# Optimization experiments

Hardware: AMD Instinct MI355X
Metric: run time of the kernel (lower is better)

## Reference

```python
import jax, jax.numpy as jnp
import numpy as np

NV, NC = 100000, 50000        # num variables, num constraints
DV, DC = 8, 16                # padded neighbor-list widths
DIN, DH = 32, 128             # init_input_dim, output_dim (=init_output_dim)
NUM_LAYERS = 3                # aggregate loop runs num_layers-1 times
DCAT = 2 * DH + DIN           # input_dim of fc_variable/fc_constraint


def setup_inputs() -> dict:
    key = jax.random.key(0)
    ks = jax.random.split(key, 10)
    w = lambda k, shape: (jax.random.normal(k, shape, jnp.float32) * 0.05)
    return {
        "x": jax.random.normal(ks[0], (NV + NC, DIN), jnp.float32),
        "var_constr_index": jax.random.randint(ks[1], (NV, DV), 0, NC, dtype=jnp.int32),
        "constr_var_index": jax.random.randint(ks[2], (NC, DC), 0, NV, dtype=jnp.int32),
        "W_init_v": w(ks[3], (DIN, DH)), "b_init_v": jnp.zeros((DH,), jnp.float32),
        "W_init_c": w(ks[4], (DIN, DH)), "b_init_c": jnp.zeros((DH,), jnp.float32),
        "W_var": w(ks[5], (DCAT, DH)), "b_var": jnp.zeros((DH,), jnp.float32),
        "W_con": w(ks[6], (DCAT, DH)), "b_con": jnp.zeros((DH,), jnp.float32),
        "W_q": w(ks[7], (2 * DH, 1)), "b_q": jnp.zeros((1,), jnp.float32),
    }


def reference(x, var_constr_index, constr_var_index,
              W_init_v, b_init_v, W_init_c, b_init_c,
              W_var, b_var, W_con, b_con, W_q, b_q):
    nv = var_constr_index.shape[0]
    xv, xc = x[:nv], x[nv:]
    # layer zero init (fc_init_variables / fc_init_constraints)
    v = xv @ W_init_v + b_init_v          # [NV, DH]
    c = xc @ W_init_c + b_init_c          # [NC, DH]
    # message-passing layers: both updates read OLD v and OLD c
    for _ in range(1, NUM_LAYERS):
        agg_c = jnp.sum(v[constr_var_index], axis=1)   # [NC, DH] gather+sum over variable neighbors
        agg_v = jnp.sum(c[var_constr_index], axis=1)   # [NV, DH] gather+sum over constraint neighbors
        c_new = jnp.concatenate([agg_c, c, xc], axis=1) @ W_con + b_con
        v_new = jnp.concatenate([agg_v, v, xv], axis=1) @ W_var + b_var
        c, v = c_new, v_new
    # embedding_Q: global sum of variable features, broadcast, concat, linear
    g = jnp.sum(v, axis=0)                             # [DH]
    q_in = jnp.concatenate([jnp.broadcast_to(g, v.shape), v], axis=1)  # [NV, 2*DH]
    return q_in @ W_q + b_q                            # [NV, 1]
```

## Files before the change

kernel.cpp:

```cpp
#include <hip/hip_runtime.h>

#define NV 100000
#define NC 50000
#define DVAR 8
#define DCON 16

using short8 = __attribute__((ext_vector_type(8))) short;
using f32x4  = __attribute__((ext_vector_type(4))) float;

__device__ __forceinline__ unsigned short f2bf(float f) {
    union { float f; unsigned int u; } v; v.f = f;
    return (unsigned short)((v.u + 0x7fffu + ((v.u >> 16) & 1u)) >> 16);
}
__device__ __forceinline__ float bflo(unsigned int u) {
    union { unsigned int u; float f; } v; v.u = u << 16; return v.f;
}
__device__ __forceinline__ float bfhi(unsigned int u) {
    union { unsigned int u; float f; } v; v.u = u & 0xffff0000u; return v.f;
}

__global__ __launch_bounds__(256) void pack_kernel(
    const float* __restrict__ Wvar, const float* __restrict__ Wcon,
    const float* __restrict__ Wiv,  const float* __restrict__ Wic,
    unsigned short* __restrict__ WbVar, unsigned short* __restrict__ WbCon,
    unsigned short* __restrict__ WbIv,  unsigned short* __restrict__ WbIc,
    float* __restrict__ S)
{
    const int tid = blockIdx.x * 256 + threadIdx.x;
    for (int i = tid; i < 9 * 128 * 32; i += gridDim.x * 256) {
        int s = i >> 12, rem = i & 4095, c = rem >> 5, k = rem & 31;
        int src = (s * 32 + k) * 128 + c;
        WbVar[i] = f2bf(Wvar[src]);
        WbCon[i] = f2bf(Wcon[src]);
    }
    for (int i = tid; i < 128 * 32; i += gridDim.x * 256) {
        int c = i >> 5, k = i & 31;
        int src = k * 128 + c;
        WbIv[i] = f2bf(Wiv[src]);
        WbIc[i] = f2bf(Wic[src]);
    }
    if (tid == 0) S[0] = 0.f;
}

__global__ __launch_bounds__(256) void init_mfma(
    const float* __restrict__ x,
    const unsigned short* __restrict__ Wb,
    const float* __restrict__ bias,
    unsigned short* __restrict__ hout, int M)
{
    const int t = threadIdx.x;
    const int lane = t & 63;
    const int w = t >> 6;
    const int lrow = lane & 15;
    const int lg = lane >> 4;
    const int wrow0 = blockIdx.x * 64 + w * 16;
    int arow = wrow0 + lrow;
    int arowc = arow < M ? arow : M - 1;

    const float4* xp = (const float4*)(x + (size_t)arowc * 32 + lg * 8);
    float4 xa = xp[0], xb = xp[1];
    short8 afr;
    afr[0] = (short)f2bf(xa.x); afr[1] = (short)f2bf(xa.y);
    afr[2] = (short)f2bf(xa.z); afr[3] = (short)f2bf(xa.w);
    afr[4] = (short)f2bf(xb.x); afr[5] = (short)f2bf(xb.y);
    afr[6] = (short)f2bf(xb.z); afr[7] = (short)f2bf(xb.w);

    #pragma unroll
    for (int ct = 0; ct < 8; ++ct) {
        int c = ct * 16 + lrow;
        short8 bfr = *(const short8*)(Wb + (size_t)c * 32 + lg * 8);
        f32x4 acc = {0.f, 0.f, 0.f, 0.f};
        acc = __builtin_amdgcn_mfma_f32_16x16x32_bf16(afr, bfr, acc, 0, 0, 0);
        float bv = bias[c];
        #pragma unroll
        for (int r = 0; r < 4; ++r) {
            int orow = wrow0 + lg * 4 + r;
            if (orow < M) hout[(size_t)orow * 128 + c] = f2bf(acc[r] + bv);
        }
    }
}

template<int DEG, bool FINAL>
__global__ __launch_bounds__(256) void layer_mfma(
    const unsigned short* hself,
    const unsigned short* __restrict__ hnb,
    const float* __restrict__ xself,
    const int* __restrict__ idx,
    const unsigned short* __restrict__ Wb,
    const float* __restrict__ bias,
    unsigned short* hout,
    const float* __restrict__ Wq, float* __restrict__ S, float* __restrict__ dotout,
    int M)
{
    __shared__ unsigned short A[64 * 136];
    __shared__ float red[4];
    const int t = threadIdx.x;
    const int r0 = blockIdx.x * 64;

    {
        const int part = t & 15;
        const int gr = t >> 4;
        #pragma unroll
        for (int rr = gr; rr < 64; rr += 16) {
            int row = r0 + rr;
            int rowc = row < M ? row : M - 1;
            int nb[DEG];
            #pragma unroll
            for (int d4 = 0; d4 < DEG / 4; ++d4)
                *(int4*)(&nb[d4 * 4]) = *(const int4*)(idx + (size_t)rowc * DEG + d4 * 4);
            float a0=0.f,a1=0.f,a2=0.f,a3=0.f,a4=0.f,a5=0.f,a6=0.f,a7=0.f;
            #pragma unroll
            for (int d = 0; d < DEG; ++d) {
                const uint4 q = *(const uint4*)(hnb + (size_t)nb[d] * 128 + part * 8);
                a0 += bflo(q.x); a1 += bfhi(q.x);
                a2 += bflo(q.y); a3 += bfhi(q.y);
                a4 += bflo(q.z); a5 += bfhi(q.z);
                a6 += bflo(q.w); a7 += bfhi(q.w);
            }
            uint4 o;
            o.x = (unsigned)f2bf(a0) | ((unsigned)f2bf(a1) << 16);
            o.y = (unsigned)f2bf(a2) | ((unsigned)f2bf(a3) << 16);
            o.z = (unsigned)f2bf(a4) | ((unsigned)f2bf(a5) << 16);
            o.w = (unsigned)f2bf(a6) | ((unsigned)f2bf(a7) << 16);
            *(uint4*)(&A[rr * 136 + part * 8]) = o;
        }
    }
    __syncthreads();

    const int lane = t & 63;
    const int w = t >> 6;
    const int lrow = lane & 15;
    const int lg = lane >> 4;
    const int wrow0 = r0 + w * 16;
    int arow = wrow0 + lrow;
    int arowc = arow < M ? arow : M - 1;

    f32x4 acc[8];
    #pragma unroll
    for (int ct = 0; ct < 8; ++ct) acc[ct] = (f32x4){0.f, 0.f, 0.f, 0.f};

    #pragma unroll
    for (int s = 0; s < 9; ++s) {
        short8 afr;
        if (s < 4) {
            afr = *(const short8*)(&A[(w * 16 + lrow) * 136 + s * 32 + lg * 8]);
        } else if (s < 8) {
            afr = *(const short8*)(hself + (size_t)arowc * 128 + (s - 4) * 32 + lg * 8);
        } else {
            const float4* xp = (const float4*)(xself + (size_t)arowc * 32 + lg * 8);
            float4 xa = xp[0], xb = xp[1];
            afr[0] = (short)f2bf(xa.x); afr[1] = (short)f2bf(xa.y);
            afr[2] = (short)f2bf(xa.z); afr[3] = (short)f2bf(xa.w);
            afr[4] = (short)f2bf(xb.x); afr[5] = (short)f2bf(xb.y);
            afr[6] = (short)f2bf(xb.z); afr[7] = (short)f2bf(xb.w);
        }
        #pragma unroll
        for (int ct = 0; ct < 8; ++ct) {
            short8 bfr = *(const short8*)(Wb + ((size_t)s * 128 + ct * 16 + lrow) * 32 + lg * 8);
            acc[ct] = __builtin_amdgcn_mfma_f32_16x16x32_bf16(afr, bfr, acc[ct], 0, 0, 0);
        }
    }

    if (!FINAL) {
        #pragma unroll
        for (int ct = 0; ct < 8; ++ct) {
            int c = ct * 16 + lrow;
            float bv = bias[c];
            #pragma unroll
            for (int r = 0; r < 4; ++r) {
                int orow = wrow0 + lg * 4 + r;
                if (orow < M) hout[(size_t)orow * 128 + c] = f2bf(acc[ct][r] + bv);
            }
        }
    } else {
        float d0[4] = {0.f, 0.f, 0.f, 0.f};
        float d1[4] = {0.f, 0.f, 0.f, 0.f};
        #pragma unroll
        for (int ct = 0; ct < 8; ++ct) {
            int c = ct * 16 + lrow;
            float bv = bias[c];
            float wq0 = Wq[c];
            float wq1 = Wq[128 + c];
            #pragma unroll
            for (int r = 0; r < 4; ++r) {
                int orow = wrow0 + lg * 4 + r;
                float val = (orow < M) ? (acc[ct][r] + bv) : 0.f;
                d0[r] += val * wq0;
                d1[r] += val * wq1;
            }
        }
        #pragma unroll
        for (int r = 0; r < 4; ++r) {
            d0[r] += __shfl_xor(d0[r], 1); d0[r] += __shfl_xor(d0[r], 2);
            d0[r] += __shfl_xor(d0[r], 4); d0[r] += __shfl_xor(d0[r], 8);
            d1[r] += __shfl_xor(d1[r], 1); d1[r] += __shfl_xor(d1[r], 2);
            d1[r] += __shfl_xor(d1[r], 4); d1[r] += __shfl_xor(d1[r], 8);
        }
        if (lrow == 0) {
            #pragma unroll
            for (int r = 0; r < 4; ++r) {
                int orow = wrow0 + lg * 4 + r;
                if (orow < M) dotout[orow] = d1[r];
            }
        }
        float tot = d0[0] + d0[1] + d0[2] + d0[3];
        tot += __shfl_xor(tot, 16);
        tot += __shfl_xor(tot, 32);
        if (lane == 0) red[w] = tot;
        __syncthreads();
        if (t == 0) atomicAdd(S, red[0] + red[1] + red[2] + red[3]);
    }
}

__global__ __launch_bounds__(256) void addout_kernel(
    float* __restrict__ outp, const float* __restrict__ S,
    const float* __restrict__ bq, int n)
{
    int i = blockIdx.x * 256 + threadIdx.x;
    if (i < n) outp[i] = outp[i] + S[0] + bq[0];
}

extern "C" void kernel_launch(void* const* d_in, const int* in_sizes, int n_in,
                              void* d_out, int out_size, void* d_ws, size_t ws_size,
                              hipStream_t stream)
{
    const float* x    = (const float*)d_in[0];
    const int*   vci  = (const int*)  d_in[1];
    const int*   cvi  = (const int*)  d_in[2];
    const float* Wiv  = (const float*)d_in[3];
    const float* biv  = (const float*)d_in[4];
    const float* Wic  = (const float*)d_in[5];
    const float* bic  = (const float*)d_in[6];
    const float* Wvar = (const float*)d_in[7];
    const float* bvar = (const float*)d_in[8];
    const float* Wcon = (const float*)d_in[9];
    const float* bcon = (const float*)d_in[10];
    const float* Wq   = (const float*)d_in[11];
    const float* bq   = (const float*)d_in[12];
    float* outp = (float*)d_out;

    unsigned short* us = (unsigned short*)d_ws;
    size_t o = 0;
    unsigned short* vA    = us + o; o += (size_t)NV * 128;
    unsigned short* cA    = us + o; o += (size_t)NC * 128;
    unsigned short* cB    = us + o; o += (size_t)NC * 128;
    unsigned short* WbVar = us + o; o += 9 * 128 * 32;
    unsigned short* WbCon = us + o; o += 9 * 128 * 32;
    unsigned short* WbIv  = us + o; o += 128 * 32;
    unsigned short* WbIc  = us + o; o += 128 * 32;
    float* S = (float*)(us + o);

    const float* xc = x + (size_t)NV * 32;

    pack_kernel<<<144, 256, 0, stream>>>(Wvar, Wcon, Wiv, Wic, WbVar, WbCon, WbIv, WbIc, S);
    init_mfma<<<(NV + 63) / 64, 256, 0, stream>>>(x,  WbIv, biv, vA, NV);
    init_mfma<<<(NC + 63) / 64, 256, 0, stream>>>(xc, WbIc, bic, cA, NC);
    layer_mfma<DCON, false><<<(NC + 63) / 64, 256, 0, stream>>>(
        cA, vA, xc, cvi, WbCon, bcon, cB, nullptr, nullptr, nullptr, NC);
    layer_mfma<DVAR, false><<<(NV + 63) / 64, 256, 0, stream>>>(
        vA, cA, x, vci, WbVar, bvar, vA, nullptr, nullptr, nullptr, NV);
    layer_mfma<DVAR, true><<<(NV + 63) / 64, 256, 0, stream>>>(
        vA, cB, x, vci, WbVar, bvar, nullptr, Wq, S, outp, NV);
    addout_kernel<<<(NV + 255) / 256, 256, 0, stream>>>(outp, S, bq, NV);
}
```

Before: 285.3 us.

## Gather neighbor aggregation directly into MFMA register fragments, dropping LDS staging

Each lane now gathers and sums neighbor rows straight into the register layout of its MFMA A-fragment, so the shared-memory tile and the block-wide barrier are no longer needed. Self and input-feature fragments are loaded up front, and their MFMAs are issued before the aggregated fragments so the matrix work can overlap the gather latency. Each lane issues four 16-byte loads per neighbor instead of one, and holding 32 float accumulators raises register pressure, which may lower occupancy.

```diff
diff --git a/kernel.cpp b/kernel.cpp
--- a/kernel.cpp
+++ b/kernel.cpp
@@ -92,68 +92,71 @@
     const float* __restrict__ Wq, float* __restrict__ S, float* __restrict__ dotout,
     int M)
 {
-    __shared__ unsigned short A[64 * 136];
     __shared__ float red[4];
     const int t = threadIdx.x;
-    const int r0 = blockIdx.x * 64;
-
-    {
-        const int part = t & 15;
-        const int gr = t >> 4;
-        #pragma unroll
-        for (int rr = gr; rr < 64; rr += 16) {
-            int row = r0 + rr;
-            int rowc = row < M ? row : M - 1;
-            int nb[DEG];
-            #pragma unroll
-            for (int d4 = 0; d4 < DEG / 4; ++d4)
-                *(int4*)(&nb[d4 * 4]) = *(const int4*)(idx + (size_t)rowc * DEG + d4 * 4);
-            float a0=0.f,a1=0.f,a2=0.f,a3=0.f,a4=0.f,a5=0.f,a6=0.f,a7=0.f;
-            #pragma unroll
-            for (int d = 0; d < DEG; ++d) {
-                const uint4 q = *(const uint4*)(hnb + (size_t)nb[d] * 128 + part * 8);
-                a0 += bflo(q.x); a1 += bfhi(q.x);
-                a2 += bflo(q.y); a3 += bfhi(q.y);
-                a4 += bflo(q.z); a5 += bfhi(q.z);
-                a6 += bflo(q.w); a7 += bfhi(q.w);
-            }
-            uint4 o;
-            o.x = (unsigned)f2bf(a0) | ((unsigned)f2bf(a1) << 16);
-            o.y = (unsigned)f2bf(a2) | ((unsigned)f2bf(a3) << 16);
-            o.z = (unsigned)f2bf(a4) | ((unsigned)f2bf(a5) << 16);
-            o.w = (unsigned)f2bf(a6) | ((unsigned)f2bf(a7) << 16);
-            *(uint4*)(&A[rr * 136 + part * 8]) = o;
-        }
-    }
-    __syncthreads();
-
     const int lane = t & 63;
     const int w = t >> 6;
     const int lrow = lane & 15;
     const int lg = lane >> 4;
-    const int wrow0 = r0 + w * 16;
-    int arow = wrow0 + lrow;
-    int arowc = arow < M ? arow : M - 1;
+    const int wrow0 = blockIdx.x * 64 + w * 16;
+    const int arow = wrow0 + lrow;
+    const int arowc = arow < M ? arow : M - 1;
+
+    int nb[DEG];
+    #pragma unroll
+    for (int d4 = 0; d4 < DEG / 4; ++d4)
+        *(int4*)(&nb[d4 * 4]) = *(const int4*)(idx + (size_t)arowc * DEG + d4 * 4);
+
+    short8 sfr[4];
+    #pragma unroll
+    for (int s = 0; s < 4; ++s)
+        sfr[s] = *(const short8*)(hself + (size_t)arowc * 128 + s * 32 + lg * 8);
+    short8 xfr;
+    {
+        const float4* xp = (const float4*)(xself + (size_t)arowc * 32 + lg * 8);
+        float4 xa = xp[0], xb = xp[1];
+        xfr[0] = (short)f2bf(xa.x); xfr[1] = (short)f2bf(xa.y);
+        xfr[2] = (short)f2bf(xa.z); xfr[3] = (short)f2bf(xa.w);
+        xfr[4] = (short)f2bf(xb.x); xfr[5] = (short)f2bf(xb.y);
+        xfr[6] = (short)f2bf(xb.z); xfr[7] = (short)f2bf(xb.w);
+    }
+
+    float ag[4][8];
+    #pragma unroll
+    for (int s = 0; s < 4; ++s)
+        #pragma unroll
+        for (int j = 0; j < 8; ++j) ag[s][j] = 0.f;
+    #pragma unroll
+    for (int d = 0; d < DEG; ++d) {
+        const unsigned short* rp = hnb + (size_t)nb[d] * 128 + lg * 8;
+        #pragma unroll
+        for (int s = 0; s < 4; ++s) {
+            const uint4 q = *(const uint4*)(rp + s * 32);
+            ag[s][0] += bflo(q.x); ag[s][1] += bfhi(q.x);
+            ag[s][2] += bflo(q.y); ag[s][3] += bfhi(q.y);
+            ag[s][4] += bflo(q.z); ag[s][5] += bfhi(q.z);
+            ag[s][6] += bflo(q.w); ag[s][7] += bfhi(q.w);
+        }
+    }
 
     f32x4 acc[8];
     #pragma unroll
     for (int ct = 0; ct < 8; ++ct) acc[ct] = (f32x4){0.f, 0.f, 0.f, 0.f};
 
     #pragma unroll
-    for (int s = 0; s < 9; ++s) {
+    for (int s = 4; s < 9; ++s) {
+        short8 afr = (s < 8) ? sfr[s - 4] : xfr;
+        #pragma unroll
+        for (int ct = 0; ct < 8; ++ct) {
+            short8 bfr = *(const short8*)(Wb + ((size_t)s * 128 + ct * 16 + lrow) * 32 + lg * 8);
+            acc[ct] = __builtin_amdgcn_mfma_f32_16x16x32_bf16(afr, bfr, acc[ct], 0, 0, 0);
+        }
+    }
+    #pragma unroll
+    for (int s = 0; s < 4; ++s) {
         short8 afr;
-        if (s < 4) {
-            afr = *(const short8*)(&A[(w * 16 + lrow) * 136 + s * 32 + lg * 8]);
-        } else if (s < 8) {
-            afr = *(const short8*)(hself + (size_t)arowc * 128 + (s - 4) * 32 + lg * 8);
-        } else {
-            const float4* xp = (const float4*)(xself + (size_t)arowc * 32 + lg * 8);
-            float4 xa = xp[0], xb = xp[1];
-            afr[0] = (short)f2bf(xa.x); afr[1] = (short)f2bf(xa.y);
-            afr[2] = (short)f2bf(xa.z); afr[3] = (short)f2bf(xa.w);
-            afr[4] = (short)f2bf(xb.x); afr[5] = (short)f2bf(xb.y);
-            afr[6] = (short)f2bf(xb.z); afr[7] = (short)f2bf(xb.w);
-        }
+        #pragma unroll
+        for (int j = 0; j < 8; ++j) afr[j] = (short)f2bf(ag[s][j]);
         #pragma unroll
         for (int ct = 0; ct < 8; ++ct) {
             short8 bfr = *(const short8*)(Wb + ((size_t)s * 128 + ct * 16 + lrow) * 32 + lg * 8);
```

After: 313.4 us. 1.1x slower.
